# Performance work log

Hardware: AMD Instinct MI355X
Metric: run time of the kernel (lower is better)

## Reference

```python
import jax, jax.numpy as jnp
import numpy as np

N_NODES = 100000
N_EDGES = 1600000
IN_CH = 64
HID = 64
OUT = 2


def sage_conv(x, src, dst, W_agg, W_root, b):
    # PyG SAGEConv (mean aggr): out = lin_l(mean_{j in N(i)} x_j) + lin_r(x_i)
    n = x.shape[0]
    msgs = x[src]                                        # [E, F] gather
    agg = jax.ops.segment_sum(msgs, dst, num_segments=n)  # [N, F] scatter-add
    cnt = jax.ops.segment_sum(jnp.ones((src.shape[0], 1), x.dtype), dst, num_segments=n)
    agg = agg / jnp.maximum(cnt, 1)                      # mean; isolated nodes -> 0
    return agg @ W_agg + x @ W_root + b


def setup_inputs() -> dict:
    key = jax.random.key(0)
    ks = jax.random.split(key, 8)
    s = lambda f: 1.0 / np.sqrt(f)
    x = jax.random.normal(ks[0], (N_NODES, IN_CH), dtype=jnp.float32)
    edge_index = jax.random.randint(ks[1], (2, N_EDGES), 0, N_NODES, dtype=jnp.int64)
    return {
        "x": x,
        "edge_index": edge_index,
        "W1_agg": jax.random.normal(ks[2], (IN_CH, HID), dtype=jnp.float32) * s(IN_CH),
        "W1_root": jax.random.normal(ks[3], (IN_CH, HID), dtype=jnp.float32) * s(IN_CH),
        "b1": jnp.zeros((HID,), jnp.float32),
        "W2_agg": jax.random.normal(ks[4], (HID, HID), dtype=jnp.float32) * s(HID),
        "W2_root": jax.random.normal(ks[5], (HID, HID), dtype=jnp.float32) * s(HID),
        "b2": jnp.zeros((HID,), jnp.float32),
        "W_lin": jax.random.normal(ks[6], (HID, OUT), dtype=jnp.float32) * s(HID),
        "b_lin": jnp.zeros((OUT,), jnp.float32),
    }


def reference(x, edge_index, W1_agg, W1_root, b1, W2_agg, W2_root, b2, W_lin, b_lin):
    src, dst = edge_index[0], edge_index[1]
    h = jax.nn.relu(sage_conv(x, src, dst, W1_agg, W1_root, b1))   # dropout = identity (eval)
    h = jax.nn.relu(sage_conv(h, src, dst, W2_agg, W2_root, b2))
    return h @ W_lin + b_lin
```

## Files before the change

### kernel.cpp

```cpp
#include <hip/hip_runtime.h>
#include <hip/hip_bf16.h>

#define FEAT 64
#define CHUNK 8192
#define MAX_NB 1024

typedef __attribute__((ext_vector_type(8))) short bf16x8;
typedef __attribute__((ext_vector_type(4))) float f32x4;
typedef __attribute__((ext_vector_type(2))) float f32x2;

__device__ __forceinline__ float bflo2f(unsigned int u) {
    union { unsigned int u; float f; } v; v.u = u << 16; return v.f;
}
__device__ __forceinline__ float bfhi2f(unsigned int u) {
    union { unsigned int u; float f; } v; v.u = u & 0xffff0000u; return v.f;
}
__device__ __forceinline__ unsigned short f2bf(float f) {
    union { float f; unsigned int u; } v; v.f = f;
    unsigned int u = v.u;
    u += 0x7fffu + ((u >> 16) & 1u);
    return (unsigned short)(u >> 16);
}
__device__ __forceinline__ f32x2 bfpair(unsigned int u) {
    f32x2 r; r.x = bflo2f(u & 0xffffu); r.y = bfhi2f(u); return r;
}

__global__ __launch_bounds__(256) void prep_kernel(
    const unsigned short* __restrict__ xh, const int* __restrict__ ei32,
    const void* __restrict__ w1a, const void* __restrict__ w1r,
    const void* __restrict__ b1,  const void* __restrict__ w2a,
    const void* __restrict__ w2r, const void* __restrict__ b2,
    const void* __restrict__ wl,  const void* __restrict__ bl,
    float* __restrict__ wbuf, unsigned short* __restrict__ Wt,
    int* __restrict__ flags, const void* __restrict__ x_in,
    unsigned short* __restrict__ x16, int n8) {
    __shared__ int cnt_bf, cnt_nz;
    int tid = threadIdx.x;
    if (tid == 0) { cnt_bf = 0; cnt_nz = 0; }
    __syncthreads();
    unsigned short h = xh[tid * 2];
    int e = (h >> 7) & 0xFF;
    if (e >= 110 && e <= 132) atomicAdd(&cnt_bf, 1);
    if (ei32[tid * 2 + 1] != 0) atomicAdd(&cnt_nz, 1);
    __syncthreads();
    int f0 = (cnt_bf >= 128) ? 1 : 0;
    if (blockIdx.x == 0 && tid == 0) {
        flags[0] = f0;
        flags[1] = (cnt_nz < 8) ? 1 : 0;
    }
    int i = blockIdx.x * 256 + tid;
    if (i < 16642) {
        const void* src; int off;
        if      (i < 4096)  { src = w1a; off = i; }
        else if (i < 8192)  { src = w1r; off = i - 4096; }
        else if (i < 8256)  { src = b1;  off = i - 8192; }
        else if (i < 12352) { src = w2a; off = i - 8256; }
        else if (i < 16448) { src = w2r; off = i - 12352; }
        else if (i < 16512) { src = b2;  off = i - 16448; }
        else if (i < 16640) { src = wl;  off = i - 16512; }
        else                { src = bl;  off = i - 16640; }
        float v = f0 ? bflo2f(((const unsigned short*)src)[off])
                     : ((const float*)src)[off];
        wbuf[i] = v;
        unsigned short hv = f2bf(v);
        if (i < 4096)                      Wt[(off & 63) * 128 + (off >> 6)] = hv;
        else if (i < 8192)                 Wt[(off & 63) * 128 + 64 + (off >> 6)] = hv;
        else if (i >= 8256 && i < 12352)   Wt[8192 + (off & 63) * 128 + (off >> 6)] = hv;
        else if (i >= 12352 && i < 16448)  Wt[8192 + (off & 63) * 128 + 64 + (off >> 6)] = hv;
    }
    if (!f0 && i < n8) {
        float4 a = ((const float4*)x_in)[2 * i];
        float4 b = ((const float4*)x_in)[2 * i + 1];
        uint4 o;
        o.x = (unsigned int)f2bf(a.x) | ((unsigned int)f2bf(a.y) << 16);
        o.y = (unsigned int)f2bf(a.z) | ((unsigned int)f2bf(a.w) << 16);
        o.z = (unsigned int)f2bf(b.x) | ((unsigned int)f2bf(b.y) << 16);
        o.w = (unsigned int)f2bf(b.z) | ((unsigned int)f2bf(b.w) << 16);
        ((uint4*)x16)[i] = o;
    }
}

__global__ __launch_bounds__(256) void p1_hist_kernel(
    const int* __restrict__ ei32, int* __restrict__ hist,
    int E, int N, int NB, int EC, const int* __restrict__ flags) {
    __shared__ int lh[MAX_NB];
    int tid = threadIdx.x, c = blockIdx.x;
    for (int i = tid; i < NB; i += 256) lh[i] = 0;
    __syncthreads();
    int idx64 = flags[1];
    long base = (long)c * CHUNK;
#pragma unroll 4
    for (int j = 0; j < CHUNK / 256; ++j) {
        long e = base + j * 256 + tid;
        if (e < E) {
            int d = idx64 ? ei32[2 * ((long)E + e)] : ei32[(long)E + e];
            if ((unsigned)d < (unsigned)N)
                atomicAdd(&lh[d >> 8], 1);
        }
    }
    __syncthreads();
    for (int k = tid; k < NB; k += 256) hist[(long)k * EC + c] = lh[k];
}

__global__ __launch_bounds__(256) void scan1_kernel(const int* __restrict__ in,
                                                    int* __restrict__ out,
                                                    int* __restrict__ blocksum, int n) {
    int tid = threadIdx.x;
    int base = blockIdx.x * 2048 + tid * 8;
    int v[8];
    int tsum = 0;
#pragma unroll
    for (int i = 0; i < 8; ++i) {
        v[i] = (base + i < n) ? in[base + i] : 0;
        tsum += v[i];
    }
    int lane = tid & 63;
    int x = tsum;
#pragma unroll
    for (int off = 1; off < 64; off <<= 1) {
        int y = __shfl_up(x, off);
        if (lane >= off) x += y;
    }
    __shared__ int wsum[4];
    int wave = tid >> 6;
    if (lane == 63) wsum[wave] = x;
    __syncthreads();
    int woff = 0;
#pragma unroll
    for (int w = 0; w < 4; ++w) if (w < wave) woff += wsum[w];
    int run = woff + x - tsum;
#pragma unroll
    for (int i = 0; i < 8; ++i) {
        if (base + i < n) out[base + i] = run;
        run += v[i];
    }
    if (tid == 255) blocksum[blockIdx.x] = woff + x;
}

__global__ void scan3_kernel(int* __restrict__ out, const int* __restrict__ blocksum, int n) {
    int i = blockIdx.x * 256 + threadIdx.x;
    if (i >= n) return;
    int nb = i >> 11;
    int pre = 0;
    for (int b = 0; b < nb; ++b) pre += blocksum[b];
    out[i] += pre;
}

__global__ __launch_bounds__(256) void p3_scatter_kernel(
    const int* __restrict__ ei32, const int* __restrict__ hscan,
    int* __restrict__ bkt, int E, int N, int NB, int EC,
    const int* __restrict__ flags) {
    __shared__ int lh[MAX_NB];
    int tid = threadIdx.x, c = blockIdx.x;
    for (int i = tid; i < NB; i += 256) lh[i] = 0;
    __syncthreads();
    int idx64 = flags[1];
    long base = (long)c * CHUNK;
#pragma unroll 4
    for (int j = 0; j < CHUNK / 256; ++j) {
        long e = base + j * 256 + tid;
        if (e < E) {
            int s = idx64 ? ei32[2 * e]             : ei32[e];
            int d = idx64 ? ei32[2 * ((long)E + e)] : ei32[(long)E + e];
            if ((unsigned)d < (unsigned)N) {
                if ((unsigned)s >= (unsigned)N) s = 0;
                int k = d >> 8;
                int r = atomicAdd(&lh[k], 1);
                bkt[hscan[(long)k * EC + c] + r] = s | ((d & 255) << 20);
            }
        }
    }
}

__global__ __launch_bounds__(256) void p4_build_kernel(
    const int* __restrict__ bkt, const int* __restrict__ hscan, const int* __restrict__ hist,
    int* __restrict__ offs, int* __restrict__ cnt, int* __restrict__ srcs,
    int E, int N, int NB, int EC) {
    int k = blockIdx.x, tid = threadIdx.x;
    int start = hscan[(long)k * EC];
    int end = (k + 1 < NB) ? hscan[(long)(k + 1) * EC]
                           : (hscan[(long)NB * EC - 1] + hist[(long)NB * EC - 1]);
    __shared__ int lc[256], lheads[256], wsum[4];
    lc[tid] = 0;
    __syncthreads();
    for (int e = start + tid; e < end; e += 256)
        atomicAdd(&lc[(bkt[e] >> 20) & 255], 1);
    __syncthreads();
    int cv = lc[tid];
    int lane = tid & 63, wave = tid >> 6;
    int x = cv;
#pragma unroll
    for (int off = 1; off < 64; off <<= 1) {
        int y = __shfl_up(x, off);
        if (lane >= off) x += y;
    }
    if (lane == 63) wsum[wave] = x;
    __syncthreads();
    int woff = 0;
#pragma unroll
    for (int w = 0; w < 4; ++w) if (w < wave) woff += wsum[w];
    int excl = woff + x - cv;
    int gnode = k * 256 + tid;
    if (gnode < N) { offs[gnode] = start + excl; cnt[gnode] = cv; }
    lheads[tid] = excl;
    __syncthreads();
    for (int e = start + tid; e < end; e += 256) {
        int p = bkt[e];
        int d8 = (p >> 20) & 255;
        int pos = start + atomicAdd(&lheads[d8], 1);
        srcs[pos] = p & 0xFFFFF;
    }
}

__global__ __launch_bounds__(256) void aggregate_kernel(
    const void* __restrict__ feat_raw, const unsigned short* __restrict__ feat_ws,
    const int* __restrict__ srcs,
    const int* __restrict__ offs, const int* __restrict__ cnt,
    unsigned short* __restrict__ agg16, int N, const int* __restrict__ flags) {
    const unsigned short* feat16 = flags[0] ? (const unsigned short*)feat_raw : feat_ws;
    int tid = threadIdx.x;
    int lane = tid & 63;
    int wave = tid >> 6;
    int g = lane >> 3;
    int li = lane & 7;
    int node = (blockIdx.x * 4 + wave) * 8 + g;
    if (node >= N) return;
    int start = offs[node];
    int deg = cnt[node];
    f32x2 a0 = {0.f, 0.f}, a1 = a0, a2 = a0, a3 = a0;
    int j = 0;
    for (; j + 4 <= deg; j += 4) {
        int s0 = srcs[start + j];
        int s1 = srcs[start + j + 1];
        int s2 = srcs[start + j + 2];
        int s3 = srcs[start + j + 3];
        uint4 u0 = *(const uint4*)(feat16 + (size_t)s0 * FEAT + 8 * li);
        uint4 u1 = *(const uint4*)(feat16 + (size_t)s1 * FEAT + 8 * li);
        uint4 u2 = *(const uint4*)(feat16 + (size_t)s2 * FEAT + 8 * li);
        uint4 u3 = *(const uint4*)(feat16 + (size_t)s3 * FEAT + 8 * li);
        a0 += bfpair(u0.x); a1 += bfpair(u0.y); a2 += bfpair(u0.z); a3 += bfpair(u0.w);
        a0 += bfpair(u1.x); a1 += bfpair(u1.y); a2 += bfpair(u1.z); a3 += bfpair(u1.w);
        a0 += bfpair(u2.x); a1 += bfpair(u2.y); a2 += bfpair(u2.z); a3 += bfpair(u2.w);
        a0 += bfpair(u3.x); a1 += bfpair(u3.y); a2 += bfpair(u3.z); a3 += bfpair(u3.w);
    }
    for (; j < deg; ++j) {
        int s = srcs[start + j];
        uint4 u = *(const uint4*)(feat16 + (size_t)s * FEAT + 8 * li);
        a0 += bfpair(u.x); a1 += bfpair(u.y); a2 += bfpair(u.z); a3 += bfpair(u.w);
    }
    float inv = 1.0f / (float)(deg > 0 ? deg : 1);
    uint4 o;
    o.x = (unsigned)f2bf(a0.x * inv) | ((unsigned)f2bf(a0.y * inv) << 16);
    o.y = (unsigned)f2bf(a1.x * inv) | ((unsigned)f2bf(a1.y * inv) << 16);
    o.z = (unsigned)f2bf(a2.x * inv) | ((unsigned)f2bf(a2.y * inv) << 16);
    o.w = (unsigned)f2bf(a3.x * inv) | ((unsigned)f2bf(a3.y * inv) << 16);
    *(uint4*)(agg16 + (size_t)node * FEAT + 8 * li) = o;
}

__global__ __launch_bounds__(256) void sage_gemm_kernel(
    const unsigned short* __restrict__ agg16,
    const void* __restrict__ root_raw, const unsigned short* __restrict__ root_ws,
    const unsigned short* __restrict__ Wt, const float* __restrict__ bias,
    unsigned short* __restrict__ out16, int N,
    const float* __restrict__ wl, const float* __restrict__ bl,
    void* __restrict__ out_final, const int* __restrict__ flags, int root_sel) {

    const unsigned short* root16 =
        (root_sel && !flags[0]) ? root_ws : (const unsigned short*)root_raw;

    __shared__ unsigned short A_l[64][136];
    __shared__ unsigned short B_l[64][136];

    int tid = threadIdx.x;
    int blk = blockIdx.x;

#pragma unroll
    for (int i = 0; i < 4; ++i) {
        int ch = tid + i * 256;
        int n = ch >> 4, kc = ch & 15;
        *(uint4*)&B_l[n][kc * 8] = *(const uint4*)(Wt + n * 128 + kc * 8);
    }
#pragma unroll
    for (int i = 0; i < 4; ++i) {
        int ch = tid + i * 256;
        int r = ch >> 4, c = ch & 15;
        int row = blk * 64 + r;
        uint4 u = make_uint4(0, 0, 0, 0);
        if (row < N)
            u = (c < 8) ? ((const uint4*)(agg16 + (size_t)row * FEAT))[c]
                        : ((const uint4*)(root16 + (size_t)row * FEAT))[c - 8];
        *(uint4*)&A_l[r][c * 8] = u;
    }
    __syncthreads();

    int lane = tid & 63;
    int wave = tid >> 6;
    int r0 = wave * 16;
    int m = lane & 15, quad = lane >> 4;

    f32x4 acc0 = {0.f, 0.f, 0.f, 0.f};
    f32x4 acc1 = acc0, acc2 = acc0, acc3 = acc0;

#pragma unroll
    for (int k0 = 0; k0 < 128; k0 += 32) {
        bf16x8 a = *(const bf16x8*)&A_l[r0 + m][k0 + quad * 8];
        bf16x8 b0 = *(const bf16x8*)&B_l[ 0 + m][k0 + quad * 8];
        bf16x8 b1 = *(const bf16x8*)&B_l[16 + m][k0 + quad * 8];
        bf16x8 b2 = *(const bf16x8*)&B_l[32 + m][k0 + quad * 8];
        bf16x8 b3 = *(const bf16x8*)&B_l[48 + m][k0 + quad * 8];
        acc0 = __builtin_amdgcn_mfma_f32_16x16x32_bf16(a, b0, acc0, 0, 0, 0);
        acc1 = __builtin_amdgcn_mfma_f32_16x16x32_bf16(a, b1, acc1, 0, 0, 0);
        acc2 = __builtin_amdgcn_mfma_f32_16x16x32_bf16(a, b2, acc2, 0, 0, 0);
        acc3 = __builtin_amdgcn_mfma_f32_16x16x32_bf16(a, b3, acc3, 0, 0, 0);
    }
    __syncthreads();

#pragma unroll
    for (int c = 0; c < 4; ++c) {
        f32x4 av = (c == 0) ? acc0 : (c == 1) ? acc1 : (c == 2) ? acc2 : acc3;
        float bv = bias[c * 16 + m];
#pragma unroll
        for (int reg = 0; reg < 4; ++reg) {
            float v = fmaxf(av[reg] + bv, 0.f);
            A_l[r0 + quad * 4 + reg][c * 16 + m] = f2bf(v);
        }
    }
    __syncthreads();

    if (out16) {
#pragma unroll
        for (int i = 0; i < 2; ++i) {
            int ch = tid + i * 256;
            int r = ch >> 3, c = ch & 7;
            int row = blk * 64 + r;
            if (row < N)
                ((uint4*)(out16 + (size_t)row * FEAT))[c] = *(const uint4*)&A_l[r][c * 8];
        }
    }

    if (wl) {
        int r = tid >> 2, part = tid & 3;
        int row = blk * 64 + r;
        if (row < N) {
            float p0 = 0.f, p1 = 0.f;
#pragma unroll
            for (int j = 0; j < 16; ++j) {
                int f = part * 16 + j;
                float v = bflo2f(A_l[r][f]);
                p0 += v * wl[f * 2 + 0];
                p1 += v * wl[f * 2 + 1];
            }
            p0 += __shfl_down(p0, 2, 4); p0 += __shfl_down(p0, 1, 4);
            p1 += __shfl_down(p1, 2, 4); p1 += __shfl_down(p1, 1, 4);
            if (part == 0) {
                p0 += bl[0];
                p1 += bl[1];
                if (flags[0]) {
                    unsigned int o = ((unsigned int)f2bf(p1) << 16) | (unsigned int)f2bf(p0);
                    ((unsigned int*)out_final)[row] = o;
                } else {
                    ((float2*)out_final)[row] = make_float2(p0, p1);
                }
            }
        }
    }
}

extern "C" void kernel_launch(void* const* d_in, const int* in_sizes, int n_in,
                              void* d_out, int out_size, void* d_ws, size_t ws_size,
                              hipStream_t stream) {
    const void* x_in = d_in[0];
    const int*  ei32 = (const int*)d_in[1];

    int N = in_sizes[0] / FEAT;
    int E = in_sizes[1] / 2;
    int NB = (N + 255) >> 8;
    int EC = (E + CHUNK - 1) / CHUNK;
    int HN = NB * EC;

    unsigned short* x16   = (unsigned short*)d_ws;
    unsigned short* h16   = x16 + (size_t)N * FEAT;
    unsigned short* agg16 = h16 + (size_t)N * FEAT;
    unsigned short* Wt    = agg16 + (size_t)N * FEAT;
    float*          wbuf  = (float*)(Wt + 16384);
    int*            hist  = (int*)(wbuf + 16704);
    int*            hscan = hist + HN;
    int*            bsum  = hscan + HN;
    int*            flags = bsum + 1024;
    int*            offs  = flags + 16;
    int*            cnt   = offs + N;
    int*            bkt   = cnt + N;
    int*            srcs  = bkt + E;

    float* b1_32 = wbuf + 8192;
    float* b2_32 = wbuf + 16448;
    float* wl32  = wbuf + 16512;
    float* bl32  = wbuf + 16640;

    int n8 = N * FEAT / 8;
    int pBlocks = (n8 + 255) / 256;
    if (pBlocks < 66) pBlocks = 66;
    prep_kernel<<<pBlocks, 256, 0, stream>>>(
        (const unsigned short*)x_in, ei32,
        d_in[2], d_in[3], d_in[4], d_in[5], d_in[6], d_in[7], d_in[8], d_in[9],
        wbuf, Wt, flags, x_in, x16, n8);

    p1_hist_kernel<<<EC, 256, 0, stream>>>(ei32, hist, E, N, NB, EC, flags);
    int sB = (HN + 2047) / 2048;
    scan1_kernel<<<sB, 256, 0, stream>>>(hist, hscan, bsum, HN);
    scan3_kernel<<<(HN + 255) / 256, 256, 0, stream>>>(hscan, bsum, HN);
    p3_scatter_kernel<<<EC, 256, 0, stream>>>(ei32, hscan, bkt, E, N, NB, EC, flags);
    p4_build_kernel<<<NB, 256, 0, stream>>>(bkt, hscan, hist, offs, cnt, srcs, E, N, NB, EC);

    int aBlocks = (N + 31) / 32;
    int gBlocks = (N + 63) / 64;

    aggregate_kernel<<<aBlocks, 256, 0, stream>>>(x_in, x16, srcs, offs, cnt, agg16, N, flags);
    sage_gemm_kernel<<<gBlocks, 256, 0, stream>>>(agg16, x_in, x16, Wt, b1_32, h16, N,
                                                  nullptr, nullptr, nullptr, flags, 1);

    aggregate_kernel<<<aBlocks, 256, 0, stream>>>(h16, h16, srcs, offs, cnt, agg16, N, flags);
    sage_gemm_kernel<<<gBlocks, 256, 0, stream>>>(agg16, h16, h16, Wt + 8192, b2_32, nullptr, N,
                                                  wl32, bl32, d_out, flags, 0);
}
```

Measured before the change: 230.7 us.

## Fuse prep with histogram, fold scan fixup into consumers, unroll gather by eight

Merges the weight/feature prep kernel with the per-chunk destination histogram kernel, and drops the separate scan fixup pass by having scatter and build kernels add block-sum prefixes on the fly. Scatter now seeds its shared-memory counters with absolute offsets, which removes a global hscan read per edge. The aggregation gather loop is unrolled to eight neighbours to put more loads in flight. The cost is serial block-sum loops inside the consumers and extra register pressure in the aggregation kernel.

```diff
diff --git a/kernel.cpp b/kernel.cpp
--- a/kernel.cpp
+++ b/kernel.cpp
@@ -25,7 +25,7 @@
     f32x2 r; r.x = bflo2f(u & 0xffffu); r.y = bfhi2f(u); return r;
 }
 
-__global__ __launch_bounds__(256) void prep_kernel(
+__global__ __launch_bounds__(256) void prep_p1_kernel(
     const unsigned short* __restrict__ xh, const int* __restrict__ ei32,
     const void* __restrict__ w1a, const void* __restrict__ w1r,
     const void* __restrict__ b1,  const void* __restrict__ w2a,
@@ -33,22 +33,27 @@
     const void* __restrict__ wl,  const void* __restrict__ bl,
     float* __restrict__ wbuf, unsigned short* __restrict__ Wt,
     int* __restrict__ flags, const void* __restrict__ x_in,
-    unsigned short* __restrict__ x16, int n8) {
+    unsigned short* __restrict__ x16, int n8,
+    int* __restrict__ hist, int E, int N, int NB, int EC) {
+    __shared__ int lh[MAX_NB];
     __shared__ int cnt_bf, cnt_nz;
     int tid = threadIdx.x;
+    int c = blockIdx.x;
+    if (c >= EC && c >= 66 && (long)c * 256 >= n8) return;
     if (tid == 0) { cnt_bf = 0; cnt_nz = 0; }
     __syncthreads();
-    unsigned short h = xh[tid * 2];
-    int e = (h >> 7) & 0xFF;
-    if (e >= 110 && e <= 132) atomicAdd(&cnt_bf, 1);
-    if (ei32[tid * 2 + 1] != 0) atomicAdd(&cnt_nz, 1);
-    __syncthreads();
-    int f0 = (cnt_bf >= 128) ? 1 : 0;
-    if (blockIdx.x == 0 && tid == 0) {
-        flags[0] = f0;
-        flags[1] = (cnt_nz < 8) ? 1 : 0;
-    }
-    int i = blockIdx.x * 256 + tid;
+    {
+        unsigned short h = xh[tid * 2];
+        int e = (h >> 7) & 0xFF;
+        if (e >= 110 && e <= 132) atomicAdd(&cnt_bf, 1);
+        if (ei32[tid * 2 + 1] != 0) atomicAdd(&cnt_nz, 1);
+    }
+    __syncthreads();
+    int f0    = (cnt_bf >= 128) ? 1 : 0;
+    int idx64 = (cnt_nz < 8) ? 1 : 0;
+    if (c == 0 && tid == 0) { flags[0] = f0; flags[1] = idx64; }
+
+    int i = c * 256 + tid;
     if (i < 16642) {
         const void* src; int off;
         if      (i < 4096)  { src = w1a; off = i; }
@@ -78,28 +83,22 @@
         o.w = (unsigned int)f2bf(b.z) | ((unsigned int)f2bf(b.w) << 16);
         ((uint4*)x16)[i] = o;
     }
-}
-
-__global__ __launch_bounds__(256) void p1_hist_kernel(
-    const int* __restrict__ ei32, int* __restrict__ hist,
-    int E, int N, int NB, int EC, const int* __restrict__ flags) {
-    __shared__ int lh[MAX_NB];
-    int tid = threadIdx.x, c = blockIdx.x;
-    for (int i = tid; i < NB; i += 256) lh[i] = 0;
-    __syncthreads();
-    int idx64 = flags[1];
-    long base = (long)c * CHUNK;
+    if (c < EC) {
+        for (int k = tid; k < NB; k += 256) lh[k] = 0;
+        __syncthreads();
+        long base = (long)c * CHUNK;
 #pragma unroll 4
-    for (int j = 0; j < CHUNK / 256; ++j) {
-        long e = base + j * 256 + tid;
-        if (e < E) {
-            int d = idx64 ? ei32[2 * ((long)E + e)] : ei32[(long)E + e];
-            if ((unsigned)d < (unsigned)N)
-                atomicAdd(&lh[d >> 8], 1);
+        for (int j = 0; j < CHUNK / 256; ++j) {
+            long e = base + j * 256 + tid;
+            if (e < E) {
+                int d = idx64 ? ei32[2 * ((long)E + e)] : ei32[(long)E + e];
+                if ((unsigned)d < (unsigned)N)
+                    atomicAdd(&lh[d >> 8], 1);
+            }
         }
-    }
-    __syncthreads();
-    for (int k = tid; k < NB; k += 256) hist[(long)k * EC + c] = lh[k];
+        __syncthreads();
+        for (int k = tid; k < NB; k += 256) hist[(long)k * EC + c] = lh[k];
+    }
 }
 
 __global__ __launch_bounds__(256) void scan1_kernel(const int* __restrict__ in,
@@ -137,22 +136,23 @@
     if (tid == 255) blocksum[blockIdx.x] = woff + x;
 }
 
-__global__ void scan3_kernel(int* __restrict__ out, const int* __restrict__ blocksum, int n) {
-    int i = blockIdx.x * 256 + threadIdx.x;
-    if (i >= n) return;
-    int nb = i >> 11;
+__device__ __forceinline__ int fold_scan(const int* __restrict__ hscan,
+                                         const int* __restrict__ bsum, long idx) {
+    int nb = (int)(idx >> 11);
     int pre = 0;
-    for (int b = 0; b < nb; ++b) pre += blocksum[b];
-    out[i] += pre;
+    for (int b = 0; b < nb; ++b) pre += bsum[b];
+    return hscan[idx] + pre;
 }
 
 __global__ __launch_bounds__(256) void p3_scatter_kernel(
     const int* __restrict__ ei32, const int* __restrict__ hscan,
+    const int* __restrict__ bsum,
     int* __restrict__ bkt, int E, int N, int NB, int EC,
     const int* __restrict__ flags) {
     __shared__ int lh[MAX_NB];
     int tid = threadIdx.x, c = blockIdx.x;
-    for (int i = tid; i < NB; i += 256) lh[i] = 0;
+    for (int k = tid; k < NB; k += 256)
+        lh[k] = fold_scan(hscan, bsum, (long)k * EC + c);
     __syncthreads();
     int idx64 = flags[1];
     long base = (long)c * CHUNK;
@@ -164,22 +164,22 @@
             int d = idx64 ? ei32[2 * ((long)E + e)] : ei32[(long)E + e];
             if ((unsigned)d < (unsigned)N) {
                 if ((unsigned)s >= (unsigned)N) s = 0;
-                int k = d >> 8;
-                int r = atomicAdd(&lh[k], 1);
-                bkt[hscan[(long)k * EC + c] + r] = s | ((d & 255) << 20);
+                int pos = atomicAdd(&lh[d >> 8], 1);
+                bkt[pos] = s | ((d & 255) << 20);
             }
         }
     }
 }
 
 __global__ __launch_bounds__(256) void p4_build_kernel(
-    const int* __restrict__ bkt, const int* __restrict__ hscan, const int* __restrict__ hist,
+    const int* __restrict__ bkt, const int* __restrict__ hscan,
+    const int* __restrict__ bsum, const int* __restrict__ hist,
     int* __restrict__ offs, int* __restrict__ cnt, int* __restrict__ srcs,
     int E, int N, int NB, int EC) {
     int k = blockIdx.x, tid = threadIdx.x;
-    int start = hscan[(long)k * EC];
-    int end = (k + 1 < NB) ? hscan[(long)(k + 1) * EC]
-                           : (hscan[(long)NB * EC - 1] + hist[(long)NB * EC - 1]);
+    int start = fold_scan(hscan, bsum, (long)k * EC);
+    int end = (k + 1 < NB) ? fold_scan(hscan, bsum, (long)(k + 1) * EC)
+                           : (fold_scan(hscan, bsum, (long)NB * EC - 1) + hist[(long)NB * EC - 1]);
     __shared__ int lc[256], lheads[256], wsum[4];
     lc[tid] = 0;
     __syncthreads();
@@ -229,19 +229,31 @@
     int deg = cnt[node];
     f32x2 a0 = {0.f, 0.f}, a1 = a0, a2 = a0, a3 = a0;
     int j = 0;
-    for (; j + 4 <= deg; j += 4) {
+    for (; j + 8 <= deg; j += 8) {
         int s0 = srcs[start + j];
         int s1 = srcs[start + j + 1];
         int s2 = srcs[start + j + 2];
         int s3 = srcs[start + j + 3];
+        int s4 = srcs[start + j + 4];
+        int s5 = srcs[start + j + 5];
+        int s6 = srcs[start + j + 6];
+        int s7 = srcs[start + j + 7];
         uint4 u0 = *(const uint4*)(feat16 + (size_t)s0 * FEAT + 8 * li);
         uint4 u1 = *(const uint4*)(feat16 + (size_t)s1 * FEAT + 8 * li);
         uint4 u2 = *(const uint4*)(feat16 + (size_t)s2 * FEAT + 8 * li);
         uint4 u3 = *(const uint4*)(feat16 + (size_t)s3 * FEAT + 8 * li);
+        uint4 u4 = *(const uint4*)(feat16 + (size_t)s4 * FEAT + 8 * li);
+        uint4 u5 = *(const uint4*)(feat16 + (size_t)s5 * FEAT + 8 * li);
+        uint4 u6 = *(const uint4*)(feat16 + (size_t)s6 * FEAT + 8 * li);
+        uint4 u7 = *(const uint4*)(feat16 + (size_t)s7 * FEAT + 8 * li);
         a0 += bfpair(u0.x); a1 += bfpair(u0.y); a2 += bfpair(u0.z); a3 += bfpair(u0.w);
         a0 += bfpair(u1.x); a1 += bfpair(u1.y); a2 += bfpair(u1.z); a3 += bfpair(u1.w);
         a0 += bfpair(u2.x); a1 += bfpair(u2.y); a2 += bfpair(u2.z); a3 += bfpair(u2.w);
         a0 += bfpair(u3.x); a1 += bfpair(u3.y); a2 += bfpair(u3.z); a3 += bfpair(u3.w);
+        a0 += bfpair(u4.x); a1 += bfpair(u4.y); a2 += bfpair(u4.z); a3 += bfpair(u4.w);
+        a0 += bfpair(u5.x); a1 += bfpair(u5.y); a2 += bfpair(u5.z); a3 += bfpair(u5.w);
+        a0 += bfpair(u6.x); a1 += bfpair(u6.y); a2 += bfpair(u6.z); a3 += bfpair(u6.w);
+        a0 += bfpair(u7.x); a1 += bfpair(u7.y); a2 += bfpair(u7.z); a3 += bfpair(u7.w);
     }
     for (; j < deg; ++j) {
         int s = srcs[start + j];
@@ -399,18 +411,17 @@
 
     int n8 = N * FEAT / 8;
     int pBlocks = (n8 + 255) / 256;
+    if (pBlocks < EC) pBlocks = EC;
     if (pBlocks < 66) pBlocks = 66;
-    prep_kernel<<<pBlocks, 256, 0, stream>>>(
+    prep_p1_kernel<<<pBlocks, 256, 0, stream>>>(
         (const unsigned short*)x_in, ei32,
         d_in[2], d_in[3], d_in[4], d_in[5], d_in[6], d_in[7], d_in[8], d_in[9],
-        wbuf, Wt, flags, x_in, x16, n8);
-
-    p1_hist_kernel<<<EC, 256, 0, stream>>>(ei32, hist, E, N, NB, EC, flags);
+        wbuf, Wt, flags, x_in, x16, n8, hist, E, N, NB, EC);
+
     int sB = (HN + 2047) / 2048;
     scan1_kernel<<<sB, 256, 0, stream>>>(hist, hscan, bsum, HN);
-    scan3_kernel<<<(HN + 255) / 256, 256, 0, stream>>>(hscan, bsum, HN);
-    p3_scatter_kernel<<<EC, 256, 0, stream>>>(ei32, hscan, bkt, E, N, NB, EC, flags);
-    p4_build_kernel<<<NB, 256, 0, stream>>>(bkt, hscan, hist, offs, cnt, srcs, E, N, NB, EC);
+    p3_scatter_kernel<<<EC, 256, 0, stream>>>(ei32, hscan, bsum, bkt, E, N, NB, EC, flags);
+    p4_build_kernel<<<NB, 256, 0, stream>>>(bkt, hscan, bsum, hist, offs, cnt, srcs, E, N, NB, EC);
 
     int aBlocks = (N + 31) / 32;
     int gBlocks = (N + 63) / 64;
```

Result: no change. 234.5 us (+1.6%).
